# Optimization experiments

Hardware: AMD Instinct MI355X
Metric: run time of the kernel (lower is better)

The kernel has to match this reference:

```python
import math
import jax, jax.numpy as jnp
import numpy as np

LOG2PI = math.log(2.0 * math.pi)


def _log_density_sum(mean, logvar, sample):
    # Gaussian log-density, summed over the trailing feature dim.
    # mean/logvar/sample broadcast against each other.
    inv_sigma = jnp.exp(-logvar)
    tmp = (sample - mean) * inv_sigma
    return jnp.sum(-0.5 * (tmp * tmp + 2.0 * logvar + LOG2PI), axis=-1)


def setup_inputs() -> dict:
    key = jax.random.key(0)
    ks = jax.random.split(key, 6)
    B, T, DF, DZ = 128, 32, 256, 128
    return {
        "f_mean":   jax.random.normal(ks[0], (B, DF), dtype=jnp.float32),
        "f_logvar": jax.random.normal(ks[1], (B, DF), dtype=jnp.float32),
        "f_sample": jax.random.normal(ks[2], (B, DF), dtype=jnp.float32),
        "z_mean":   jax.random.normal(ks[3], (B, T, DZ), dtype=jnp.float32),
        "z_logvar": jax.random.normal(ks[4], (B, T, DZ), dtype=jnp.float32),
        "z_sample": jax.random.normal(ks[5], (B, T, DZ), dtype=jnp.float32),
        "num_train": 50000,
    }


def reference(f_mean, f_logvar, f_sample, z_mean, z_logvar, z_sample, num_train):
    B = f_mean.shape[0]
    log_norm = math.log(B) + math.log(num_train)

    # f pairwise: sample index i vs mean index j -> [B_i, B_j]
    # (original repeats this identically over every step t)
    logq_f_sum = _log_density_sum(
        f_mean[None, :, :], f_logvar[None, :, :], f_sample[:, None, :]
    )  # [B, B]

    # z pairwise per step: transpose to [T, B, D], then [T, B_i, B_j]
    zt_mean = jnp.transpose(z_mean, (1, 0, 2))
    zt_logvar = jnp.transpose(z_logvar, (1, 0, 2))
    zt_sample = jnp.transpose(z_sample, (1, 0, 2))
    logq_z_sum = _log_density_sum(
        zt_mean[:, None, :, :], zt_logvar[:, None, :, :], zt_sample[:, :, None, :]
    )  # [T, B, B]

    # concatenating f and z components along the feature dim then summing
    # equals summing the per-component feature sums
    logq_fz_sum = logq_f_sum[None, :, :] + logq_z_sum  # [T, B, B]

    logq_f = jax.nn.logsumexp(logq_f_sum, axis=1) - log_norm          # [B]
    logq_z = jax.nn.logsumexp(logq_z_sum, axis=2) - log_norm          # [T, B]
    logq_fz = jax.nn.logsumexp(logq_fz_sum, axis=2) - log_norm        # [T, B]

    mi_fz = jnp.mean(jax.nn.relu(logq_fz - logq_f[None, :] - logq_z))
    return mi_fz
```

## Files before the change

kernel.cpp:

```cpp
#include <hip/hip_runtime.h>

#define LOG2PI 1.8378770664093453f



__device__ __forceinline__ float waveReduceSum(float v) {
#pragma unroll
    for (int o = 32; o > 0; o >>= 1) v += __shfl_down(v, o, 64);
    return v;
}

__device__ __forceinline__ float waveReduceMax(float v) {
#pragma unroll
    for (int o = 32; o > 0; o >>= 1) v = fmaxf(v, __shfl_down(v, o, 64));
    return v;
}

__device__ __forceinline__ float blockReduceSum(float v, float* sh) {
    int lane = threadIdx.x & 63, wid = threadIdx.x >> 6, nw = blockDim.x >> 6;
    v = waveReduceSum(v);
    __syncthreads();
    if (lane == 0) sh[wid] = v;
    __syncthreads();
    float r = sh[0];
    for (int w = 1; w < nw; ++w) r += sh[w];
    return r;
}

__device__ __forceinline__ float blockReduceMax(float v, float* sh) {
    int lane = threadIdx.x & 63, wid = threadIdx.x >> 6, nw = blockDim.x >> 6;
    v = waveReduceMax(v);
    __syncthreads();
    if (lane == 0) sh[wid] = v;
    __syncthreads();
    float r = sh[0];
    for (int w = 1; w < nw; ++w) r = fmaxf(r, sh[w]);
    return r;
}

__device__ __forceinline__ float4 blockMax4(float4 v, float4* sh) {
#pragma unroll
    for (int o = 32; o > 0; o >>= 1) {
        v.x = fmaxf(v.x, __shfl_down(v.x, o, 64));
        v.y = fmaxf(v.y, __shfl_down(v.y, o, 64));
        v.z = fmaxf(v.z, __shfl_down(v.z, o, 64));
        v.w = fmaxf(v.w, __shfl_down(v.w, o, 64));
    }
    int lane = threadIdx.x & 63, wid = threadIdx.x >> 6;
    __syncthreads();
    if (lane == 0) sh[wid] = v;
    __syncthreads();
    float4 a = sh[0], b = sh[1];
    return make_float4(fmaxf(a.x, b.x), fmaxf(a.y, b.y),
                       fmaxf(a.z, b.z), fmaxf(a.w, b.w));
}

__device__ __forceinline__ float4 blockSum4(float4 v, float4* sh) {
#pragma unroll
    for (int o = 32; o > 0; o >>= 1) {
        v.x += __shfl_down(v.x, o, 64);
        v.y += __shfl_down(v.y, o, 64);
        v.z += __shfl_down(v.z, o, 64);
        v.w += __shfl_down(v.w, o, 64);
    }
    int lane = threadIdx.x & 63, wid = threadIdx.x >> 6;
    __syncthreads();
    if (lane == 0) sh[wid] = v;
    __syncthreads();
    float4 a = sh[0], b = sh[1];
    return make_float4(a.x + b.x, a.y + b.y, a.z + b.z, a.w + b.w);
}

__global__ void tz_ker(const float* __restrict__ zm, const float* __restrict__ zlv,
                       float2* __restrict__ zme) {
    __shared__ float sm[32][33];
    __shared__ float se[32][33];
    int blk = blockIdx.x;
    int t = blk >> 4;
    int bt = (blk >> 2) & 3;
    int dt = blk & 3;
    int tx = threadIdx.x & 31;
    int ty = threadIdx.x >> 5;
    int b0 = bt * 32, d0 = dt * 32;
#pragma unroll
    for (int k = 0; k < 4; ++k) {
        int bl = ty + k * 8;
        int idx = (b0 + bl) * 4096 + t * 128 + d0 + tx;
        sm[bl][tx] = zm[idx];
        se[bl][tx] = expf(-2.f * zlv[idx]);
    }
    __syncthreads();
#pragma unroll
    for (int k = 0; k < 4; ++k) {
        int dl = ty + k * 8;
        zme[(t * 128 + d0 + dl) * 128 + b0 + tx] =
            make_float2(sm[tx][dl], se[tx][dl]);
    }
}

__global__ void tf_ker(const float* __restrict__ fm, const float* __restrict__ flv,
                       float2* __restrict__ fme) {
    __shared__ float sm[32][33];
    __shared__ float se[32][33];
    int blk = blockIdx.x;
    int bt = blk >> 3;
    int dt = blk & 7;
    int tx = threadIdx.x & 31;
    int ty = threadIdx.x >> 5;
    int b0 = bt * 32, d0 = dt * 32;
#pragma unroll
    for (int k = 0; k < 4; ++k) {
        int bl = ty + k * 8;
        int idx = (b0 + bl) * 256 + d0 + tx;
        sm[bl][tx] = fm[idx];
        se[bl][tx] = expf(-2.f * flv[idx]);
    }
    __syncthreads();
#pragma unroll
    for (int k = 0; k < 4; ++k) {
        int dl = ty + k * 8;
        fme[(d0 + dl) * 128 + b0 + tx] = make_float2(sm[tx][dl], se[tx][dl]);
    }
}

__global__ void sums_ker(const float* __restrict__ zlv, const float* __restrict__ flv,
                         float* __restrict__ cz, float* __restrict__ cf) {
    __shared__ float sh[2];
    int blk = blockIdx.x, tid = threadIdx.x;
    if (blk < 4096) {
        int b = blk >> 5, t = blk & 31;
        float s = 2.f * zlv[b * 4096 + t * 128 + tid];
        s = blockReduceSum(s, sh);
        if (tid == 0) cz[t * 128 + b] = s;
    } else {
        int b = blk - 4096;
        float s = 2.f * (flv[b * 256 + tid] + flv[b * 256 + 128 + tid]);
        s = blockReduceSum(s, sh);
        if (tid == 0) cf[b] = s;
    }
}

__global__ void fker(const float* __restrict__ fs, const float2* __restrict__ fme,
                     const float* __restrict__ cf,
                     float* __restrict__ F, float* __restrict__ lse_f) {
    __shared__ float s_fs[256];
    __shared__ float sh[2];
    int i = blockIdx.x, j = threadIdx.x;
    s_fs[j] = fs[i * 256 + j];
    s_fs[j + 128] = fs[i * 256 + 128 + j];
    __syncthreads();
    float acc = 0.f;
#pragma unroll 8
    for (int d = 0; d < 256; ++d) {
        float2 me = fme[d * 128 + j];
        float df = s_fs[d] - me.x;
        acc = fmaf(df * df, me.y, acc);
    }
    float Fij = -0.5f * (acc + cf[j] + 256.f * LOG2PI);
    F[i * 128 + j] = Fij;
    float m = blockReduceMax(Fij, sh);
    float s = blockReduceSum(expf(Fij - m), sh);
    if (j == 0) lse_f[i] = m + logf(s);
}

__global__ void zker(const float* __restrict__ zs, const float2* __restrict__ zme,
                     const float* __restrict__ cz, const float* __restrict__ F,
                     const float* __restrict__ lse_f, const int* __restrict__ num_train,
                     float* __restrict__ val) {
    __shared__ float4 s_zs[128];
    __shared__ float4 sh4[2];
    int blk = blockIdx.x;
    int t = blk >> 5;
    int i0 = (blk & 31) * 4;
    int j = threadIdx.x;

    float* s_zs_f = (float*)s_zs;
#pragma unroll
    for (int k = 0; k < 4; ++k)
        s_zs_f[j * 4 + k] = zs[(i0 + k) * 4096 + t * 128 + j];
    __syncthreads();

    const float2* zmt = zme + t * 16384;
    float4 acc = make_float4(0.f, 0.f, 0.f, 0.f);
#pragma unroll 8
    for (int d = 0; d < 128; ++d) {
        float2 me = zmt[d * 128 + j];
        float4 z = s_zs[d];
        float d0 = z.x - me.x; acc.x = fmaf(d0 * d0, me.y, acc.x);
        float d1 = z.y - me.x; acc.y = fmaf(d1 * d1, me.y, acc.y);
        float d2 = z.z - me.x; acc.z = fmaf(d2 * d2, me.y, acc.z);
        float d3 = z.w - me.x; acc.w = fmaf(d3 * d3, me.y, acc.w);
    }

    float base = -0.5f * (cz[t * 128 + j] + 128.f * LOG2PI);
    float4 rz = make_float4(-0.5f * acc.x + base, -0.5f * acc.y + base,
                            -0.5f * acc.z + base, -0.5f * acc.w + base);
    float4 fz = make_float4(rz.x + F[(i0 + 0) * 128 + j],
                            rz.y + F[(i0 + 1) * 128 + j],
                            rz.z + F[(i0 + 2) * 128 + j],
                            rz.w + F[(i0 + 3) * 128 + j]);

    float4 mz = blockMax4(rz, sh4);
    float4 e = make_float4(expf(rz.x - mz.x), expf(rz.y - mz.y),
                           expf(rz.z - mz.z), expf(rz.w - mz.w));
    float4 sz = blockSum4(e, sh4);
    float4 mf = blockMax4(fz, sh4);
    e = make_float4(expf(fz.x - mf.x), expf(fz.y - mf.y),
                    expf(fz.z - mf.z), expf(fz.w - mf.w));
    float4 sf = blockSum4(e, sh4);

    if (j == 0) {
        float log_norm = logf(128.f * (float)num_train[0]);
        float lz[4] = {mz.x + logf(sz.x), mz.y + logf(sz.y),
                       mz.z + logf(sz.z), mz.w + logf(sz.w)};
        float lfz[4] = {mf.x + logf(sf.x), mf.y + logf(sf.y),
                        mf.z + logf(sf.z), mf.w + logf(sf.w)};
#pragma unroll
        for (int k = 0; k < 4; ++k) {
            float v = lfz[k] - lse_f[i0 + k] - lz[k] + log_norm;
            val[t * 128 + i0 + k] = v > 0.f ? v : 0.f;
        }
    }
}

__global__ void rker(const float* __restrict__ val, float* __restrict__ out) {
    __shared__ float sh[4];
    float s = 0.f;
    for (int k = threadIdx.x; k < 4096; k += 256) s += val[k];
    s = blockReduceSum(s, sh);
    if (threadIdx.x == 0) out[0] = s / 4096.f;
}

extern "C" void kernel_launch(void* const* d_in, const int* in_sizes, int n_in,
                              void* d_out, int out_size, void* d_ws, size_t ws_size,
                              hipStream_t stream) {
    const float* f_mean    = (const float*)d_in[0];
    const float* f_logvar  = (const float*)d_in[1];
    const float* f_sample  = (const float*)d_in[2];
    const float* z_mean    = (const float*)d_in[3];
    const float* z_logvar  = (const float*)d_in[4];
    const float* z_sample  = (const float*)d_in[5];
    const int*   num_train = (const int*)d_in[6];
    float* out = (float*)d_out;

    float* ws    = (float*)d_ws;
    float2* zme  = (float2*)ws;
    float2* fme  = (float2*)(ws + 1048576);
    float*  cz   = ws + 1048576 + 65536;
    float*  cf   = cz + 4096;
    float*  F    = cf + 128;
    float*  lse_f= F + 16384;
    float*  val  = lse_f + 128;

    tz_ker<<<512, 256, 0, stream>>>(z_mean, z_logvar, zme);
    tf_ker<<<32, 256, 0, stream>>>(f_mean, f_logvar, fme);
    sums_ker<<<4224, 128, 0, stream>>>(z_logvar, f_logvar, cz, cf);
    fker<<<128, 128, 0, stream>>>(f_sample, fme, cf, F, lse_f);
    zker<<<1024, 128, 0, stream>>>(z_sample, zme, cz, F, lse_f, num_train, val);
    rker<<<1, 256, 0, stream>>>(val, out);
}
```

Measured before the change: 106.5 us.

## Merge prep kernels, split fker feature loop, fold final reduction via atomics

Combines the z/f transpose kernels and the logvar-sum kernel into one prep launch that also zeroes the output. fker now uses 256 threads, splitting the feature dimension in half and combining the partial sums through shared memory. The separate final reduction kernel is removed; zker accumulates its contribution straight into the output with atomicAdd. This cuts the launch count from six to three and the per-launch overhead, at the cost of a float atomic ordering that is no longer deterministic.

```diff
diff --git a/kernel.cpp b/kernel.cpp
--- a/kernel.cpp
+++ b/kernel.cpp
@@ -71,72 +71,77 @@
     return make_float4(a.x + b.x, a.y + b.y, a.z + b.z, a.w + b.w);
 }
 
-__global__ void tz_ker(const float* __restrict__ zm, const float* __restrict__ zlv,
-                       float2* __restrict__ zme) {
-    __shared__ float sm[32][33];
-    __shared__ float se[32][33];
+#define NB_TZ 512
+#define NB_TF 32
+#define NB_ZS 2048
+#define NB_FS 128
+
+__global__ void prep(const float* __restrict__ zm, const float* __restrict__ zlv,
+                     const float* __restrict__ fm, const float* __restrict__ flv,
+                     float2* __restrict__ zme, float2* __restrict__ fme,
+                     float* __restrict__ cz, float* __restrict__ cf,
+                     float* __restrict__ out) {
+    __shared__ float S[2 * 32 * 33];
+    float (*sm)[33] = (float(*)[33])S;
+    float (*se)[33] = (float(*)[33])(S + 32 * 33);
     int blk = blockIdx.x;
-    int t = blk >> 4;
-    int bt = (blk >> 2) & 3;
-    int dt = blk & 3;
-    int tx = threadIdx.x & 31;
-    int ty = threadIdx.x >> 5;
-    int b0 = bt * 32, d0 = dt * 32;
-#pragma unroll
-    for (int k = 0; k < 4; ++k) {
-        int bl = ty + k * 8;
-        int idx = (b0 + bl) * 4096 + t * 128 + d0 + tx;
-        sm[bl][tx] = zm[idx];
-        se[bl][tx] = expf(-2.f * zlv[idx]);
-    }
-    __syncthreads();
-#pragma unroll
-    for (int k = 0; k < 4; ++k) {
-        int dl = ty + k * 8;
-        zme[(t * 128 + d0 + dl) * 128 + b0 + tx] =
-            make_float2(sm[tx][dl], se[tx][dl]);
-    }
-}
-
-__global__ void tf_ker(const float* __restrict__ fm, const float* __restrict__ flv,
-                       float2* __restrict__ fme) {
-    __shared__ float sm[32][33];
-    __shared__ float se[32][33];
-    int blk = blockIdx.x;
-    int bt = blk >> 3;
-    int dt = blk & 7;
-    int tx = threadIdx.x & 31;
-    int ty = threadIdx.x >> 5;
-    int b0 = bt * 32, d0 = dt * 32;
-#pragma unroll
-    for (int k = 0; k < 4; ++k) {
-        int bl = ty + k * 8;
-        int idx = (b0 + bl) * 256 + d0 + tx;
-        sm[bl][tx] = fm[idx];
-        se[bl][tx] = expf(-2.f * flv[idx]);
-    }
-    __syncthreads();
-#pragma unroll
-    for (int k = 0; k < 4; ++k) {
-        int dl = ty + k * 8;
-        fme[(d0 + dl) * 128 + b0 + tx] = make_float2(sm[tx][dl], se[tx][dl]);
-    }
-}
-
-__global__ void sums_ker(const float* __restrict__ zlv, const float* __restrict__ flv,
-                         float* __restrict__ cz, float* __restrict__ cf) {
-    __shared__ float sh[2];
-    int blk = blockIdx.x, tid = threadIdx.x;
-    if (blk < 4096) {
-        int b = blk >> 5, t = blk & 31;
-        float s = 2.f * zlv[b * 4096 + t * 128 + tid];
-        s = blockReduceSum(s, sh);
-        if (tid == 0) cz[t * 128 + b] = s;
+    int tid = threadIdx.x;
+
+    if (blk < NB_TZ) {
+        int t = blk >> 4, bt = (blk >> 2) & 3, dt = blk & 3;
+        int tx = tid & 31, ty = tid >> 5;
+        int b0 = bt * 32, d0 = dt * 32;
+#pragma unroll
+        for (int k = 0; k < 4; ++k) {
+            int bl = ty + k * 8;
+            int idx = (b0 + bl) * 4096 + t * 128 + d0 + tx;
+            sm[bl][tx] = zm[idx];
+            se[bl][tx] = expf(-2.f * zlv[idx]);
+        }
+        __syncthreads();
+#pragma unroll
+        for (int k = 0; k < 4; ++k) {
+            int dl = ty + k * 8;
+            zme[(t * 128 + d0 + dl) * 128 + b0 + tx] =
+                make_float2(sm[tx][dl], se[tx][dl]);
+        }
+    } else if (blk < NB_TZ + NB_TF) {
+        int r = blk - NB_TZ;
+        int bt = r >> 3, dt = r & 7;
+        int tx = tid & 31, ty = tid >> 5;
+        int b0 = bt * 32, d0 = dt * 32;
+#pragma unroll
+        for (int k = 0; k < 4; ++k) {
+            int bl = ty + k * 8;
+            int idx = (b0 + bl) * 256 + d0 + tx;
+            sm[bl][tx] = fm[idx];
+            se[bl][tx] = expf(-2.f * flv[idx]);
+        }
+        __syncthreads();
+#pragma unroll
+        for (int k = 0; k < 4; ++k) {
+            int dl = ty + k * 8;
+            fme[(d0 + dl) * 128 + b0 + tx] = make_float2(sm[tx][dl], se[tx][dl]);
+        }
+    } else if (blk < NB_TZ + NB_TF + NB_ZS) {
+        int r0 = (blk - NB_TZ - NB_TF) * 2;
+        int half = tid >> 7, lane = tid & 127;
+        int r = r0 + half;
+        int b = r >> 5, t = r & 31;
+        float v = 2.f * zlv[b * 4096 + t * 128 + lane];
+        v = waveReduceSum(v);
+        int wid = tid >> 6;
+        if ((tid & 63) == 0) S[wid] = v;
+        __syncthreads();
+        if (tid == 0)   cz[(r0 & 31) * 128 + (r0 >> 5)] = S[0] + S[1];
+        if (tid == 128) { int r1 = r0 + 1; cz[(r1 & 31) * 128 + (r1 >> 5)] = S[2] + S[3]; }
+    } else if (blk < NB_TZ + NB_TF + NB_ZS + NB_FS) {
+        int b = blk - NB_TZ - NB_TF - NB_ZS;
+        float v = 2.f * flv[b * 256 + tid];
+        v = blockReduceSum(v, S);
+        if (tid == 0) cf[b] = v;
     } else {
-        int b = blk - 4096;
-        float s = 2.f * (flv[b * 256 + tid] + flv[b * 256 + 128 + tid]);
-        s = blockReduceSum(s, sh);
-        if (tid == 0) cf[b] = s;
+        if (tid == 0) out[0] = 0.f;
     }
 }
 
@@ -144,29 +149,39 @@
                      const float* __restrict__ cf,
                      float* __restrict__ F, float* __restrict__ lse_f) {
     __shared__ float s_fs[256];
-    __shared__ float sh[2];
-    int i = blockIdx.x, j = threadIdx.x;
-    s_fs[j] = fs[i * 256 + j];
-    s_fs[j + 128] = fs[i * 256 + 128 + j];
-    __syncthreads();
+    __shared__ float part[256];
+    __shared__ float sh[4];
+    int i = blockIdx.x, tid = threadIdx.x;
+    int j = tid & 127, dh = tid >> 7;
+    s_fs[tid] = fs[i * 256 + tid];
+    __syncthreads();
+    const float2* fp = fme + dh * 128 * 128;
+    const float* ss = s_fs + dh * 128;
     float acc = 0.f;
 #pragma unroll 8
-    for (int d = 0; d < 256; ++d) {
-        float2 me = fme[d * 128 + j];
-        float df = s_fs[d] - me.x;
+    for (int d = 0; d < 128; ++d) {
+        float2 me = fp[d * 128 + j];
+        float df = ss[d] - me.x;
         acc = fmaf(df * df, me.y, acc);
     }
-    float Fij = -0.5f * (acc + cf[j] + 256.f * LOG2PI);
-    F[i * 128 + j] = Fij;
-    float m = blockReduceMax(Fij, sh);
-    float s = blockReduceSum(expf(Fij - m), sh);
-    if (j == 0) lse_f[i] = m + logf(s);
+    part[tid] = acc;
+    __syncthreads();
+    float Fij = 0.f;
+    if (dh == 0) {
+        Fij = -0.5f * (acc + part[tid + 128] + cf[j] + 256.f * LOG2PI);
+        F[i * 128 + j] = Fij;
+    }
+    float v = (dh == 0) ? Fij : -INFINITY;
+    float m = blockReduceMax(v, sh);
+    float e = (dh == 0) ? expf(Fij - m) : 0.f;
+    float s = blockReduceSum(e, sh);
+    if (tid == 0) lse_f[i] = m + logf(s);
 }
 
 __global__ void zker(const float* __restrict__ zs, const float2* __restrict__ zme,
                      const float* __restrict__ cz, const float* __restrict__ F,
                      const float* __restrict__ lse_f, const int* __restrict__ num_train,
-                     float* __restrict__ val) {
+                     float* __restrict__ out) {
     __shared__ float4 s_zs[128];
     __shared__ float4 sh4[2];
     int blk = blockIdx.x;
@@ -215,20 +230,14 @@
                        mz.z + logf(sz.z), mz.w + logf(sz.w)};
         float lfz[4] = {mf.x + logf(sf.x), mf.y + logf(sf.y),
                         mf.z + logf(sf.z), mf.w + logf(sf.w)};
+        float s = 0.f;
 #pragma unroll
         for (int k = 0; k < 4; ++k) {
             float v = lfz[k] - lse_f[i0 + k] - lz[k] + log_norm;
-            val[t * 128 + i0 + k] = v > 0.f ? v : 0.f;
-        }
-    }
-}
-
-__global__ void rker(const float* __restrict__ val, float* __restrict__ out) {
-    __shared__ float sh[4];
-    float s = 0.f;
-    for (int k = threadIdx.x; k < 4096; k += 256) s += val[k];
-    s = blockReduceSum(s, sh);
-    if (threadIdx.x == 0) out[0] = s / 4096.f;
+            s += (v > 0.f ? v : 0.f);
+        }
+        atomicAdd(out, s * (1.f / 4096.f));
+    }
 }
 
 extern "C" void kernel_launch(void* const* d_in, const int* in_sizes, int n_in,
@@ -250,12 +259,9 @@
     float*  cf   = cz + 4096;
     float*  F    = cf + 128;
     float*  lse_f= F + 16384;
-    float*  val  = lse_f + 128;
-
-    tz_ker<<<512, 256, 0, stream>>>(z_mean, z_logvar, zme);
-    tf_ker<<<32, 256, 0, stream>>>(f_mean, f_logvar, fme);
-    sums_ker<<<4224, 128, 0, stream>>>(z_logvar, f_logvar, cz, cf);
-    fker<<<128, 128, 0, stream>>>(f_sample, fme, cf, F, lse_f);
-    zker<<<1024, 128, 0, stream>>>(z_sample, zme, cz, F, lse_f, num_train, val);
-    rker<<<1, 256, 0, stream>>>(val, out);
-}
+
+    prep<<<NB_TZ + NB_TF + NB_ZS + NB_FS + 1, 256, 0, stream>>>(
+        z_mean, z_logvar, f_mean, f_logvar, zme, fme, cz, cf, out);
+    fker<<<128, 256, 0, stream>>>(f_sample, fme, cf, F, lse_f);
+    zker<<<1024, 128, 0, stream>>>(z_sample, zme, cz, F, lse_f, num_train, out);
+}
```

New measurement: 105.6 us. No clear change (-0.8%).
